# Kernel optimization log

Measured on AMD Instinct MI355X. Metric: run time of the kernel, lower is better.

The kernel has to match this reference:

```python
import jax, jax.numpy as jnp
import numpy as np

B, N, D = 16, 4096, 64
LB_TH = 0.01
L2_LAMDA = 0.001
RECONS_LAMDA = 0.2


def _xavier(key, shape):
    fan_in, fan_out = shape[0], shape[1]
    a = float(np.sqrt(6.0 / (fan_in + fan_out)))
    return jax.random.uniform(key, shape, jnp.float32, -a, a)


def setup_inputs() -> dict:
    key = jax.random.key(0)
    k1, k2, k3 = jax.random.split(key, 3)
    X = jax.random.normal(k1, (B, N, D), jnp.float32)
    r_proj = _xavier(k2, (D, D))
    incidence_m = _xavier(k3, (N, N - 1))
    return {"X": X, "r_proj": r_proj, "incidence_m": incidence_m}


def reference(X, r_proj, incidence_m):
    n = incidence_m.shape[0]
    # clamp(min=lb_th) followed by masked_fill(~(v > lb_th), 0) == keep only orig > lb_th
    w = jnp.where(incidence_m > LB_TH, incidence_m, jnp.zeros((), X.dtype))  # [N, N-1]
    # scatter each row's N-1 weights into an NxN matrix, skipping the diagonal
    rows = jnp.arange(n)[:, None]                      # [N,1]
    cols = jnp.arange(n - 1)[None, :]                  # [1,N-1]
    full_cols = cols + (cols >= rows).astype(cols.dtype)  # [N,N-1]
    W = jnp.zeros((n, n), X.dtype).at[rows, full_cols].set(w)
    # per-node projection of master node features: X @ r_proj
    X_proj = jnp.einsum('bnd,de->bne', X, r_proj)      # [B,N,D]
    # neighbor reconstruction for every node at once
    recon = jnp.einsum('ij,bjd->bid', W, X)            # [B,N,D]
    recon_err = jnp.sqrt(jnp.sum((X_proj - recon) ** 2, axis=-1))  # [B,N]
    l1 = jnp.max(jnp.abs(w), axis=1)                   # [N] (max over single-row sum == max abs)
    l2 = jnp.sqrt(jnp.sum(w ** 2, axis=1))             # [N]
    recon_loss = recon_err * RECONS_LAMDA + l1[None, :] + L2_LAMDA * l2[None, :]
    incidence_all = W + jnp.eye(n, dtype=X.dtype)
    return recon_loss, incidence_all
```

## Files before the change

### kernel.cpp

```cpp
#include <hip/hip_runtime.h>
#include <hip/hip_bf16.h>

#define BB 16
#define NN 4096
#define DD 64
#define NM1 4095

typedef __bf16 bf16x8 __attribute__((ext_vector_type(8)));
typedef float f32x4 __attribute__((ext_vector_type(4)));

typedef __attribute__((address_space(1))) const void gas_void;
typedef __attribute__((address_space(3))) void las_void;


__global__ __launch_bounds__(256) void build_kernel(
    const float* __restrict__ inc, float* __restrict__ out_inc,
    __bf16* __restrict__ A16, float* __restrict__ mxa, float* __restrict__ ssa)
{
    int t = threadIdx.x;
    int base = blockIdx.x << 12;
    int rA = (int)((unsigned)base / NM1);
    float pm0 = 0.f, ps0 = 0.f, pm1 = 0.f, ps1 = 0.f;
    #pragma unroll
    for (int j = 0; j < 16; ++j) {
        int f = base + j * 256 + t;
        int i = (int)((unsigned)f / NM1);
        int c = f - i * NM1;
        float x = inc[f];
        float w = x > 0.01f ? x : 0.f;
        int dst = f + i + (c >= i);
        out_inc[dst] = w;
        A16[dst] = (__bf16)w;
        if (i == rA) { pm0 = fmaxf(pm0, w); ps0 += w * w; }
        else         { pm1 = fmaxf(pm1, w); ps1 += w * w; }
    }
    #pragma unroll
    for (int off = 32; off; off >>= 1) {
        pm0 = fmaxf(pm0, __shfl_down(pm0, off));
        ps0 += __shfl_down(ps0, off);
        pm1 = fmaxf(pm1, __shfl_down(pm1, off));
        ps1 += __shfl_down(ps1, off);
    }
    __shared__ float sm0[4], sq0[4], sm1[4], sq1[4];
    int wid = t >> 6;
    if ((t & 63) == 0) { sm0[wid] = pm0; sq0[wid] = ps0; sm1[wid] = pm1; sq1[wid] = ps1; }
    __syncthreads();
    if (t == 0) {
        float m0v = fmaxf(fmaxf(sm0[0], sm0[1]), fmaxf(sm0[2], sm0[3]));
        float s0v = sq0[0] + sq0[1] + sq0[2] + sq0[3];
        float m1v = fmaxf(fmaxf(sm1[0], sm1[1]), fmaxf(sm1[2], sm1[3]));
        float s1v = sq1[0] + sq1[1] + sq1[2] + sq1[3];
        atomicMax((unsigned*)(mxa + rA), __float_as_uint(m0v));
        atomicAdd(ssa + rA, s0v);
        int rB = rA + 1;
        if (rB < NN) {
            atomicMax((unsigned*)(mxa + rB), __float_as_uint(m1v));
            atomicAdd(ssa + rB, s1v);
        }
    }
}

__global__ __launch_bounds__(256) void xt_kernel(
    const float* __restrict__ X, __bf16* __restrict__ XT,
    float* __restrict__ out_inc, __bf16* __restrict__ A16)
{
    __shared__ __bf16 tile[64 * 72];
    int t = threadIdx.x;
    int ntile = blockIdx.x, b = blockIdx.y;
    int n = t >> 2, q = t & 3;
    const float* src = X + ((size_t)b * NN + ntile * 64 + n) * DD + q * 16;
    #pragma unroll
    for (int v = 0; v < 4; ++v) {
        f32x4 u = *(const f32x4*)(src + v * 4);
        #pragma unroll
        for (int j = 0; j < 4; ++j) {
            int d = q * 16 + v * 4 + j;
            tile[d * 72 + n] = (__bf16)u[j];
        }
    }
    __syncthreads();
    int d = t >> 2;
    __bf16* dst = XT + ((size_t)b * DD + d) * NN + ntile * 64 + q * 16;
    *(bf16x8*)dst       = *(bf16x8*)&tile[d * 72 + q * 16];
    *(bf16x8*)(dst + 8) = *(bf16x8*)&tile[d * 72 + q * 16 + 8];
    if (b == 0 && t < 64) {
        int r = ntile * 64 + t;
        out_inc[(size_t)r * NN + r] = 1.0f;
        A16[(size_t)r * NN + r] = (__bf16)1.0f;
    }
}

__global__ __launch_bounds__(512, 2) void gemm_loss_kernel(
    const __bf16* __restrict__ A16, const __bf16* __restrict__ XT,
    const float* __restrict__ X, const float* __restrict__ rproj,
    const float* __restrict__ mxa, const float* __restrict__ ssa,
    float* __restrict__ loss)
{
    __shared__ __bf16 smem[4 * 16384];

    const int t = threadIdx.x;
    const int wave = t >> 6, lane = t & 63;
    const int quad = lane >> 4, ln = lane & 15;
    const int sr = lane >> 3, so = lane & 7;
    const int bq = wave >> 2;
    const int wr = (wave & 3) << 5;
    const int m0 = blockIdx.x * 128;
    const int b0 = blockIdx.y * 2;

    const __bf16* Abase = A16 + (size_t)m0 * NN;
    const __bf16* XTb   = XT + (size_t)b0 * DD * NN;

    f32x4 acc[2][4];
    f32x4 zero = {0.f, 0.f, 0.f, 0.f};
    #pragma unroll
    for (int mt = 0; mt < 2; ++mt)
        #pragma unroll
        for (int ct = 0; ct < 4; ++ct) acc[mt][ct] = zero;

    auto stage = [&](int buf, int kt) {
        __bf16* bA = smem + buf * 16384;
        __bf16* bX = bA + 8192;
        const int k0 = kt << 6;
        #pragma unroll
        for (int p = 0; p < 2; ++p) {
            const int r0 = (p << 6) + (wave << 3);
            const int r  = r0 + sr;
            const int og = so ^ (r & 7);
            __builtin_amdgcn_global_load_lds(
                (gas_void*)(Abase + (size_t)r * NN + k0 + (og << 3)),
                (las_void*)(bA + r0 * 64), 16, 0, 0);
            __builtin_amdgcn_global_load_lds(
                (gas_void*)(XTb + (size_t)r * NN + k0 + (og << 3)),
                (las_void*)(bX + r0 * 64), 16, 0, 0);
        }
    };

    auto compute = [&](int buf) {
        const __bf16* bA = smem + buf * 16384;
        const __bf16* bX = bA + 8192 + (bq << 12);
        __builtin_amdgcn_s_setprio(1);
        #pragma unroll
        for (int kk = 0; kk < 64; kk += 32) {
            const int oc = (kk >> 3) + quad;
            bf16x8 af[2], bfr[4];
            #pragma unroll
            for (int mt = 0; mt < 2; ++mt) {
                const int r = wr + mt * 16 + ln;
                af[mt] = *(const bf16x8*)&bA[r * 64 + ((oc ^ (r & 7)) << 3)];
            }
            #pragma unroll
            for (int ct = 0; ct < 4; ++ct) {
                const int n = ct * 16 + ln;
                bfr[ct] = *(const bf16x8*)&bX[n * 64 + ((oc ^ (n & 7)) << 3)];
            }
            #pragma unroll
            for (int mt = 0; mt < 2; ++mt)
                #pragma unroll
                for (int ct = 0; ct < 4; ++ct)
                    acc[mt][ct] = __builtin_amdgcn_mfma_f32_16x16x32_bf16(
                        af[mt], bfr[ct], acc[mt][ct], 0, 0, 0);
        }
        __builtin_amdgcn_s_setprio(0);
    };

    const int NT = NN / 64;
    stage(0, 0);
    stage(1, 1);
    stage(2, 2);
    for (int kt = 0; kt < NT - 3; ++kt) {
        asm volatile("s_waitcnt vmcnt(8)" ::: "memory");
        __builtin_amdgcn_s_barrier();
        __builtin_amdgcn_sched_barrier(0);
        compute(kt & 3);
        stage((kt + 3) & 3, kt + 3);
    }
    asm volatile("s_waitcnt vmcnt(8)" ::: "memory");
    __builtin_amdgcn_s_barrier();
    __builtin_amdgcn_sched_barrier(0);
    compute(1);
    asm volatile("s_waitcnt vmcnt(4)" ::: "memory");
    __builtin_amdgcn_s_barrier();
    __builtin_amdgcn_sched_barrier(0);
    compute(2);
    asm volatile("s_waitcnt vmcnt(0)" ::: "memory");
    __builtin_amdgcn_s_barrier();
    __builtin_amdgcn_sched_barrier(0);
    compute(3);

    __syncthreads();

    {
        const int rr = t >> 2, q = t & 3;
        #pragma unroll
        for (int bb = 0; bb < 2; ++bb) {
            const float* xs = X + ((size_t)(b0 + bb) * NN + m0 + rr) * DD + q * 16;
            __bf16* XA = smem + bb * 8192;
            #pragma unroll
            for (int v = 0; v < 2; ++v) {
                f32x4 u0 = *(const f32x4*)(xs + v * 8);
                f32x4 u1 = *(const f32x4*)(xs + v * 8 + 4);
                bf16x8 w;
                #pragma unroll
                for (int j = 0; j < 4; ++j) { w[j] = (__bf16)u0[j]; w[j + 4] = (__bf16)u1[j]; }
                const int o = (q * 2 + v) ^ (rr & 7);
                *(bf16x8*)&XA[rr * 64 + o * 8] = w;
            }
        }
        if (t < 256) {
            const int rr2 = t >> 2, q2 = t & 3;
            const float* rs = rproj + (size_t)rr2 * DD + q2 * 16;
            __bf16* R = smem + 16384;
            #pragma unroll
            for (int v = 0; v < 4; ++v) {
                f32x4 u = *(const f32x4*)(rs + v * 4);
                #pragma unroll
                for (int j = 0; j < 4; ++j) {
                    const int d = q2 * 16 + v * 4 + j;
                    float val = u[j] + (d == rr2 ? 1.0f : 0.0f);
                    R[d * 64 + (((rr2 >> 3) ^ (d & 7)) << 3) + (rr2 & 7)] = (__bf16)val;
                }
            }
        }
    }
    __syncthreads();

    #pragma unroll
    for (int mt = 0; mt < 2; ++mt)
        #pragma unroll
        for (int ct = 0; ct < 4; ++ct) acc[mt][ct] = -acc[mt][ct];

    {
        const __bf16* XA = smem + bq * 8192;
        const __bf16* R  = smem + 16384;
        #pragma unroll
        for (int kk = 0; kk < DD; kk += 32) {
            const int oc = (kk >> 3) + quad;
            bf16x8 af[2], bfr[4];
            #pragma unroll
            for (int mt = 0; mt < 2; ++mt) {
                const int r = wr + mt * 16 + ln;
                af[mt] = *(const bf16x8*)&XA[r * 64 + ((oc ^ (r & 7)) << 3)];
            }
            #pragma unroll
            for (int ct = 0; ct < 4; ++ct) {
                const int n = ct * 16 + ln;
                bfr[ct] = *(const bf16x8*)&R[n * 64 + ((oc ^ (n & 7)) << 3)];
            }
            #pragma unroll
            for (int mt = 0; mt < 2; ++mt)
                #pragma unroll
                for (int ct = 0; ct < 4; ++ct)
                    acc[mt][ct] = __builtin_amdgcn_mfma_f32_16x16x32_bf16(
                        af[mt], bfr[ct], acc[mt][ct], 0, 0, 0);
        }
    }

    #pragma unroll
    for (int mt = 0; mt < 2; ++mt) {
        #pragma unroll
        for (int rg = 0; rg < 4; ++rg) {
            float s = 0.f;
            #pragma unroll
            for (int ct = 0; ct < 4; ++ct) {
                float d = acc[mt][ct][rg];
                s += d * d;
            }
            s += __shfl_xor(s, 1);
            s += __shfl_xor(s, 2);
            s += __shfl_xor(s, 4);
            s += __shfl_xor(s, 8);
            if (ln == 0) {
                int row = m0 + wr + mt * 16 + quad * 4 + rg;
                loss[(size_t)(b0 + bq) * NN + row] =
                    0.2f * sqrtf(s) + mxa[row] + 0.001f * sqrtf(ssa[row]);
            }
        }
    }
}

extern "C" void kernel_launch(void* const* d_in, const int* in_sizes, int n_in,
                              void* d_out, int out_size, void* d_ws, size_t ws_size,
                              hipStream_t stream) {
    const float* X   = (const float*)d_in[0];
    const float* r   = (const float*)d_in[1];
    const float* inc = (const float*)d_in[2];
    float* out      = (float*)d_out;
    float* out_loss = out;
    float* out_inc  = out + (size_t)BB * NN;

    char* ws = (char*)d_ws;
    float*  mxa = (float*)ws;
    float*  ssa = (float*)(ws + 16384);
    __bf16* XT  = (__bf16*)(ws + 32768);
    __bf16* A16 = (__bf16*)(ws + 32768 + (size_t)8 * 1024 * 1024);

    hipMemsetAsync(mxa, 0, 32768, stream);

    hipLaunchKernelGGL(build_kernel, dim3(NM1), dim3(256), 0, stream,
                       inc, out_inc, A16, mxa, ssa);
    hipLaunchKernelGGL(xt_kernel, dim3(NN / 64, BB), dim3(256), 0, stream,
                       X, XT, out_inc, A16);
    hipLaunchKernelGGL(gemm_loss_kernel, dim3(NN / 128, BB / 2), dim3(512), 0, stream,
                       A16, XT, X, r, mxa, ssa, out_loss);
}
```

Before: 185.5 us.

## Load A operand directly from global into registers, stage only XT in LDS

The A16 incidence tile is no longer staged through shared memory. Each lane now loads its MFMA A fragments straight from global into registers, one k-tile ahead, in a double-buffered register set. Only the XT tile still goes through the 4-deep LDS ring, which halves the shared memory footprint and removes the A LDS writes and reads. The pipeline waitcnt schedule is rewritten to match, which adds register pressure and issues narrower, less coalesced global loads for A.

```diff
diff --git a/kernel.cpp b/kernel.cpp
--- a/kernel.cpp
+++ b/kernel.cpp
@@ -90,13 +90,15 @@
     }
 }
 
+struct ASet { bf16x8 m0k0, m0k1, m1k0, m1k1; };
+
 __global__ __launch_bounds__(512, 2) void gemm_loss_kernel(
     const __bf16* __restrict__ A16, const __bf16* __restrict__ XT,
     const float* __restrict__ X, const float* __restrict__ rproj,
     const float* __restrict__ mxa, const float* __restrict__ ssa,
     float* __restrict__ loss)
 {
-    __shared__ __bf16 smem[4 * 16384];
+    __shared__ __bf16 smem[4 * 8192];
 
     const int t = threadIdx.x;
     const int wave = t >> 6, lane = t & 63;
@@ -107,8 +109,11 @@
     const int m0 = blockIdx.x * 128;
     const int b0 = blockIdx.y * 2;
 
-    const __bf16* Abase = A16 + (size_t)m0 * NN;
-    const __bf16* XTb   = XT + (size_t)b0 * DD * NN;
+    const __bf16* XTb = XT + (size_t)b0 * DD * NN;
+    const int og = so ^ sr;
+
+    const __bf16* aA0 = A16 + (size_t)(m0 + wr + ln) * NN + quad * 8;
+    const __bf16* aA1 = aA0 + (size_t)16 * NN;
 
     f32x4 acc[2][4];
     f32x4 zero = {0.f, 0.f, 0.f, 0.f};
@@ -118,74 +123,79 @@
         for (int ct = 0; ct < 4; ++ct) acc[mt][ct] = zero;
 
     auto stage = [&](int buf, int kt) {
-        __bf16* bA = smem + buf * 16384;
-        __bf16* bX = bA + 8192;
+        __bf16* bX = smem + (buf << 13);
         const int k0 = kt << 6;
         #pragma unroll
         for (int p = 0; p < 2; ++p) {
             const int r0 = (p << 6) + (wave << 3);
             const int r  = r0 + sr;
-            const int og = so ^ (r & 7);
-            __builtin_amdgcn_global_load_lds(
-                (gas_void*)(Abase + (size_t)r * NN + k0 + (og << 3)),
-                (las_void*)(bA + r0 * 64), 16, 0, 0);
             __builtin_amdgcn_global_load_lds(
                 (gas_void*)(XTb + (size_t)r * NN + k0 + (og << 3)),
                 (las_void*)(bX + r0 * 64), 16, 0, 0);
         }
     };
 
-    auto compute = [&](int buf) {
-        const __bf16* bA = smem + buf * 16384;
-        const __bf16* bX = bA + 8192 + (bq << 12);
+    auto loada = [&](ASet& d, int kt) {
+        const __bf16* p0 = aA0 + ((size_t)kt << 6);
+        const __bf16* p1 = aA1 + ((size_t)kt << 6);
+        d.m0k0 = *(const bf16x8*)p0;
+        d.m0k1 = *(const bf16x8*)(p0 + 32);
+        d.m1k0 = *(const bf16x8*)p1;
+        d.m1k1 = *(const bf16x8*)(p1 + 32);
+    };
+
+    auto compute = [&](const ASet& s, int buf) {
+        const __bf16* bX = smem + (buf << 13) + (bq << 12);
         __builtin_amdgcn_s_setprio(1);
         #pragma unroll
-        for (int kk = 0; kk < 64; kk += 32) {
-            const int oc = (kk >> 3) + quad;
-            bf16x8 af[2], bfr[4];
-            #pragma unroll
-            for (int mt = 0; mt < 2; ++mt) {
-                const int r = wr + mt * 16 + ln;
-                af[mt] = *(const bf16x8*)&bA[r * 64 + ((oc ^ (r & 7)) << 3)];
-            }
+        for (int h = 0; h < 2; ++h) {
+            const int oc = (h << 2) + quad;
+            bf16x8 a0 = h ? s.m0k1 : s.m0k0;
+            bf16x8 a1 = h ? s.m1k1 : s.m1k0;
+            bf16x8 bfr[4];
             #pragma unroll
             for (int ct = 0; ct < 4; ++ct) {
                 const int n = ct * 16 + ln;
                 bfr[ct] = *(const bf16x8*)&bX[n * 64 + ((oc ^ (n & 7)) << 3)];
             }
             #pragma unroll
-            for (int mt = 0; mt < 2; ++mt)
-                #pragma unroll
-                for (int ct = 0; ct < 4; ++ct)
-                    acc[mt][ct] = __builtin_amdgcn_mfma_f32_16x16x32_bf16(
-                        af[mt], bfr[ct], acc[mt][ct], 0, 0, 0);
+            for (int ct = 0; ct < 4; ++ct) {
+                acc[0][ct] = __builtin_amdgcn_mfma_f32_16x16x32_bf16(
+                    a0, bfr[ct], acc[0][ct], 0, 0, 0);
+                acc[1][ct] = __builtin_amdgcn_mfma_f32_16x16x32_bf16(
+                    a1, bfr[ct], acc[1][ct], 0, 0, 0);
+            }
         }
         __builtin_amdgcn_s_setprio(0);
     };
 
-    const int NT = NN / 64;
-    stage(0, 0);
-    stage(1, 1);
-    stage(2, 2);
-    for (int kt = 0; kt < NT - 3; ++kt) {
-        asm volatile("s_waitcnt vmcnt(8)" ::: "memory");
-        __builtin_amdgcn_s_barrier();
-        __builtin_amdgcn_sched_barrier(0);
-        compute(kt & 3);
-        stage((kt + 3) & 3, kt + 3);
-    }
-    asm volatile("s_waitcnt vmcnt(8)" ::: "memory");
-    __builtin_amdgcn_s_barrier();
-    __builtin_amdgcn_sched_barrier(0);
-    compute(1);
-    asm volatile("s_waitcnt vmcnt(4)" ::: "memory");
-    __builtin_amdgcn_s_barrier();
-    __builtin_amdgcn_sched_barrier(0);
-    compute(2);
-    asm volatile("s_waitcnt vmcnt(0)" ::: "memory");
-    __builtin_amdgcn_s_barrier();
-    __builtin_amdgcn_sched_barrier(0);
-    compute(3);
+#define FENCE() asm volatile("" ::: "memory")
+#define VMCNT(N) asm volatile("s_waitcnt vmcnt(" #N ")" ::: "memory")
+#define BAR() do { __builtin_amdgcn_s_barrier(); \
+                   __builtin_amdgcn_sched_barrier(0); } while (0)
+
+    ASet af0, af1;
+    stage(0, 0); FENCE();
+    stage(1, 1); FENCE();
+    stage(2, 2); FENCE();
+    loada(af0, 0);
+
+    VMCNT(8);  BAR(); stage(3, 3); loada(af1, 1); compute(af0, 0);
+    VMCNT(12); BAR(); stage(0, 4); loada(af0, 2); compute(af1, 1);
+    for (int kt = 2; kt < 60; kt += 2) {
+        VMCNT(12); BAR(); stage((kt + 3) & 3, kt + 3);
+        loada(af1, kt + 1); compute(af0, kt & 3);
+        VMCNT(12); BAR(); stage((kt + 4) & 3, kt + 4);
+        loada(af0, kt + 2); compute(af1, (kt + 1) & 3);
+    }
+    VMCNT(12); BAR(); stage(3, 63); loada(af1, 61); compute(af0, 0);
+    VMCNT(12); BAR(); loada(af0, 62); compute(af1, 1);
+    VMCNT(10); BAR(); loada(af1, 63); compute(af0, 2);
+    VMCNT(8);  BAR(); compute(af1, 3);
+
+#undef BAR
+#undef VMCNT
+#undef FENCE
 
     __syncthreads();
 
```

New measurement: 232.1 us. 25.2% more time.

## Prefetch epilogue operands during the main loop and issue stage loads before compute

Applied to the files above, without the earlier changes.

The rproj, mxa/ssa and X tile loads needed by the loss epilogue are now issued early: at kernel start, or just before the last compute step. Their latency is meant to hide behind the main GEMM loop instead of stalling after it. The projection matrix is staged into a separate LDS buffer before the loop. The row-norm terms are read from LDS at the end. Inside the loop the next stage's async loads are issued before the current compute, to give memory more lead time. This costs extra registers and about 9KB more LDS, which may add pressure on an already large shared-memory footprint.

```diff
diff --git a/kernel.cpp b/kernel.cpp
--- a/kernel.cpp
+++ b/kernel.cpp
@@ -97,6 +97,8 @@
     float* __restrict__ loss)
 {
     __shared__ __bf16 smem[4 * 16384];
+    __shared__ __bf16 Rr[64 * 64];
+    __shared__ float  msl[256];
 
     const int t = threadIdx.x;
     const int wave = t >> 6, lane = t & 63;
@@ -109,6 +111,24 @@
 
     const __bf16* Abase = A16 + (size_t)m0 * NN;
     const __bf16* XTb   = XT + (size_t)b0 * DD * NN;
+
+#define FENCE() asm volatile("" ::: "memory")
+#define VMCNT(N) asm volatile("s_waitcnt vmcnt(" #N ")" ::: "memory")
+#define BAR() do { __builtin_amdgcn_s_barrier(); \
+                   __builtin_amdgcn_sched_barrier(0); } while (0)
+
+    float mxv = 0.f, ssv = 0.f;
+    if (t < 128) { mxv = mxa[m0 + t]; ssv = ssa[m0 + t]; }
+    f32x4 rv0, rv1, rv2, rv3;
+    const int rr2 = t >> 2, q2 = t & 3;
+    if (t < 256) {
+        const float* rs = rproj + (size_t)rr2 * DD + q2 * 16;
+        rv0 = *(const f32x4*)(rs);
+        rv1 = *(const f32x4*)(rs + 4);
+        rv2 = *(const f32x4*)(rs + 8);
+        rv3 = *(const f32x4*)(rs + 12);
+    }
+    FENCE();
 
     f32x4 acc[2][4];
     f32x4 zero = {0.f, 0.f, 0.f, 0.f};
@@ -164,41 +184,62 @@
     };
 
     const int NT = NN / 64;
-    stage(0, 0);
-    stage(1, 1);
-    stage(2, 2);
+    stage(0, 0); FENCE();
+    stage(1, 1); FENCE();
+    stage(2, 2); FENCE();
+
+    if (t < 256) {
+        #pragma unroll
+        for (int v = 0; v < 4; ++v) {
+            f32x4 u = v == 0 ? rv0 : v == 1 ? rv1 : v == 2 ? rv2 : rv3;
+            #pragma unroll
+            for (int j = 0; j < 4; ++j) {
+                const int d = q2 * 16 + v * 4 + j;
+                float val = u[j] + (d == rr2 ? 1.0f : 0.0f);
+                Rr[d * 64 + (((rr2 >> 3) ^ (d & 7)) << 3) + (rr2 & 7)] = (__bf16)val;
+            }
+        }
+    }
+
     for (int kt = 0; kt < NT - 3; ++kt) {
-        asm volatile("s_waitcnt vmcnt(8)" ::: "memory");
-        __builtin_amdgcn_s_barrier();
-        __builtin_amdgcn_sched_barrier(0);
+        VMCNT(8);
+        BAR();
+        stage((kt + 3) & 3, kt + 3);
         compute(kt & 3);
-        stage((kt + 3) & 3, kt + 3);
-    }
-    asm volatile("s_waitcnt vmcnt(8)" ::: "memory");
-    __builtin_amdgcn_s_barrier();
-    __builtin_amdgcn_sched_barrier(0);
-    compute(1);
-    asm volatile("s_waitcnt vmcnt(4)" ::: "memory");
-    __builtin_amdgcn_s_barrier();
-    __builtin_amdgcn_sched_barrier(0);
-    compute(2);
-    asm volatile("s_waitcnt vmcnt(0)" ::: "memory");
-    __builtin_amdgcn_s_barrier();
-    __builtin_amdgcn_sched_barrier(0);
-    compute(3);
-
-    __syncthreads();
-
+    }
+    VMCNT(8);  BAR(); compute(1);
+    VMCNT(4);  BAR(); compute(2);
+    VMCNT(0);  BAR();
+
+    f32x4 xa[2][2][2];
+    const int rr = t >> 2, q = t & 3;
     {
-        const int rr = t >> 2, q = t & 3;
         #pragma unroll
         for (int bb = 0; bb < 2; ++bb) {
             const float* xs = X + ((size_t)(b0 + bb) * NN + m0 + rr) * DD + q * 16;
+            #pragma unroll
+            for (int v = 0; v < 2; ++v) {
+                xa[bb][v][0] = *(const f32x4*)(xs + v * 8);
+                xa[bb][v][1] = *(const f32x4*)(xs + v * 8 + 4);
+            }
+        }
+    }
+    compute(3);
+
+#undef BAR
+#undef VMCNT
+#undef FENCE
+
+    __syncthreads();
+
+    {
+        #pragma unroll
+        for (int bb = 0; bb < 2; ++bb) {
             __bf16* XA = smem + bb * 8192;
             #pragma unroll
             for (int v = 0; v < 2; ++v) {
-                f32x4 u0 = *(const f32x4*)(xs + v * 8);
-                f32x4 u1 = *(const f32x4*)(xs + v * 8 + 4);
+                f32x4 u0 = xa[bb][v][0];
+                f32x4 u1 = xa[bb][v][1];
                 bf16x8 w;
                 #pragma unroll
                 for (int j = 0; j < 4; ++j) { w[j] = (__bf16)u0[j]; w[j + 4] = (__bf16)u1[j]; }
@@ -206,21 +247,7 @@
                 *(bf16x8*)&XA[rr * 64 + o * 8] = w;
             }
         }
-        if (t < 256) {
-            const int rr2 = t >> 2, q2 = t & 3;
-            const float* rs = rproj + (size_t)rr2 * DD + q2 * 16;
-            __bf16* R = smem + 16384;
-            #pragma unroll
-            for (int v = 0; v < 4; ++v) {
-                f32x4 u = *(const f32x4*)(rs + v * 4);
-                #pragma unroll
-                for (int j = 0; j < 4; ++j) {
-                    const int d = q2 * 16 + v * 4 + j;
-                    float val = u[j] + (d == rr2 ? 1.0f : 0.0f);
-                    R[d * 64 + (((rr2 >> 3) ^ (d & 7)) << 3) + (rr2 & 7)] = (__bf16)val;
-                }
-            }
-        }
+        if (t < 128) { msl[t] = mxv; msl[128 + t] = ssv; }
     }
     __syncthreads();
 
@@ -231,7 +258,6 @@
 
     {
         const __bf16* XA = smem + bq * 8192;
-        const __bf16* R  = smem + 16384;
         #pragma unroll
         for (int kk = 0; kk < DD; kk += 32) {
             const int oc = (kk >> 3) + quad;
@@ -244,7 +270,7 @@
             #pragma unroll
             for (int ct = 0; ct < 4; ++ct) {
                 const int n = ct * 16 + ln;
-                bfr[ct] = *(const bf16x8*)&R[n * 64 + ((oc ^ (n & 7)) << 3)];
+                bfr[ct] = *(const bf16x8*)&Rr[n * 64 + ((oc ^ (n & 7)) << 3)];
             }
             #pragma unroll
             for (int mt = 0; mt < 2; ++mt)
@@ -270,9 +296,9 @@
             s += __shfl_xor(s, 4);
             s += __shfl_xor(s, 8);
             if (ln == 0) {
-                int row = m0 + wr + mt * 16 + quad * 4 + rg;
-                loss[(size_t)(b0 + bq) * NN + row] =
-                    0.2f * sqrtf(s) + mxa[row] + 0.001f * sqrtf(ssa[row]);
+                int rloc = wr + mt * 16 + quad * 4 + rg;
+                loss[(size_t)(b0 + bq) * NN + m0 + rloc] =
+                    0.2f * sqrtf(s) + msl[rloc] + 0.001f * sqrtf(msl[128 + rloc]);
             }
         }
     }
```

Result: slower. 208.4 us (+12.4%).
